# Performance work log

Hardware: AMD Instinct MI355X
Metric: run time of the kernel (lower is better)

## Reference

```python
import jax, jax.numpy as jnp
import numpy as np

B, N, M, C = 4, 4096, 300, 1152
SA_H, SA_D = 36, 32           # linear self-attention heads / head dim
CA_H = 16                     # cross-attention heads
INNER_SA = SA_H * SA_D        # 1152
INNER_FF = int(C * 2.5)       # 2880
EPS = 1e-6


def _ln(x):
    # LayerNorm without affine, eps=1e-6
    mu = x.mean(-1, keepdims=True)
    var = x.var(-1, keepdims=True)
    return (x - mu) / jnp.sqrt(var + EPS)


def setup_inputs() -> dict:
    key = jax.random.key(0)
    ks = jax.random.split(key, 24)
    p = lambda i, shape: jax.random.normal(ks[i], shape, jnp.float32) * 0.02
    return {
        "x": jax.random.normal(ks[0], (B, N, C), jnp.float32),
        "conditioning": jax.random.normal(ks[1], (B, M, C), jnp.float32),
        "t_emb": jax.random.normal(ks[2], (B, C), jnp.float32),
        # linear self-attention (qkv has no bias)
        "w_qkv": p(3, (C, 3 * INNER_SA)),
        "w_sa_out": p(4, (INNER_SA, C)),
        "b_sa_out": jnp.zeros((C,), jnp.float32),
        # norm_cross (affine LayerNorm)
        "gamma_cross": jnp.ones((C,), jnp.float32),
        "beta_cross": jnp.zeros((C,), jnp.float32),
        # cross-attention
        "w_q": p(5, (C, C)), "b_q": jnp.zeros((C,), jnp.float32),
        "w_kv": p(6, (C, 2 * C)), "b_kv": jnp.zeros((2 * C,), jnp.float32),
        "w_co": p(7, (C, C)), "b_co": jnp.zeros((C,), jnp.float32),
        # MixFFN
        "w_fc1": p(8, (C, 2 * INNER_FF)), "b_fc1": jnp.zeros((2 * INNER_FF,), jnp.float32),
        "dw_kernel": p(9, (3, 3, 1, INNER_FF)),  # depthwise conv, HWIO
        "dw_bias": jnp.zeros((INNER_FF,), jnp.float32),
        "w_fc2": p(10, (INNER_FF, C)), "b_fc2": jnp.zeros((C,), jnp.float32),
        # adaLN modulation
        "w_ada": p(11, (C, 6 * C)), "b_ada": jnp.zeros((6 * C,), jnp.float32),
        "sst": jax.random.normal(ks[12], (6, C), jnp.float32) * 0.02,
    }


def reference(x, conditioning, t_emb, w_qkv, w_sa_out, b_sa_out,
              gamma_cross, beta_cross, w_q, b_q, w_kv, b_kv, w_co, b_co,
              w_fc1, b_fc1, dw_kernel, dw_bias, w_fc2, b_fc2,
              w_ada, b_ada, sst):
    Bx, Nx, Cx = x.shape
    ada = jax.nn.silu(t_emb) @ w_ada + b_ada          # (B, 6C)
    ada = sst[None] + ada.reshape(Bx, 6, Cx)          # (B, 6, C)
    shift_sa, scale_sa, gate_sa, shift_ff, scale_ff, gate_ff = (
        ada[:, 0], ada[:, 1], ada[:, 2], ada[:, 3], ada[:, 4], ada[:, 5])

    # --- modulated linear self-attention (ReLU kernel) ---
    xn = _ln(x) * (1.0 + scale_sa[:, None]) + shift_sa[:, None]
    qkv = (xn @ w_qkv).reshape(Bx, Nx, 3, SA_H, SA_D)
    q = jax.nn.relu(qkv[:, :, 0])
    k = jax.nn.relu(qkv[:, :, 1])
    v = qkv[:, :, 2]
    kv = jnp.einsum('bnhd,bnhe->bhde', k, v)                  # (B,H,D,D)
    out = jnp.einsum('bnhd,bhde->bnhe', q, kv)                # (B,N,H,D)
    denom = jnp.einsum('bnhd,bhd->bnh', q, k.sum(1)) + 1e-6   # (B,N,H)
    out = (out / denom[..., None]).reshape(Bx, Nx, INNER_SA)
    x = x + gate_sa[:, None] * (out @ w_sa_out + b_sa_out)

    # --- cross-attention (softmax) ---
    xc = _ln(x) * gamma_cross + beta_cross
    hd = Cx // CA_H
    qc = (xc @ w_q + b_q).reshape(Bx, Nx, CA_H, hd)
    kvc = (conditioning @ w_kv + b_kv).reshape(Bx, M, 2, CA_H, hd)
    kc, vc = kvc[:, :, 0], kvc[:, :, 1]
    attn = jnp.einsum('bnhd,bmhd->bhnm', qc, kc) * (hd ** -0.5)
    attn = jax.nn.softmax(attn, axis=-1)
    oc = jnp.einsum('bhnm,bmhd->bnhd', attn, vc).reshape(Bx, Nx, Cx)
    x = x + oc @ w_co + b_co

    # --- modulated GLU-dwconv FFN ---
    xn = _ln(x) * (1.0 + scale_ff[:, None]) + shift_ff[:, None]
    gv = xn @ w_fc1 + b_fc1
    gate, val = gv[..., :INNER_FF], gv[..., INNER_FF:]
    h = jax.nn.silu(gate) * val
    hw = int(round(Nx ** 0.5))
    h = h.reshape(Bx, hw, hw, INNER_FF)                       # NHWC
    h = jax.lax.conv_general_dilated(
        h, dw_kernel, window_strides=(1, 1), padding='SAME',
        dimension_numbers=('NHWC', 'HWIO', 'NHWC'),
        feature_group_count=INNER_FF) + dw_bias
    h = h.reshape(Bx, Nx, INNER_FF)
    x = x + gate_ff[:, None] * (h @ w_fc2 + b_fc2)
    return x
```

## Files before the change

### kernel.cpp

```cpp
#include <hip/hip_runtime.h>

typedef __bf16 bf16_t;
typedef __attribute__((ext_vector_type(8))) __bf16 bf16x8;
typedef __attribute__((ext_vector_type(4))) __bf16 bf16x4;
typedef __attribute__((ext_vector_type(4))) float f32x4;

#define DEVINL __device__ __forceinline__

DEVINL void gload16(const void* g, void* l) {
  __builtin_amdgcn_global_load_lds(
      (const __attribute__((address_space(1))) void*)g,
      (__attribute__((address_space(3))) void*)l, 16, 0, 0);
}

template <int OUT>
__global__ __launch_bounds__(512) void gemm256r(
    const bf16_t* __restrict__ A, const bf16_t* __restrict__ Bt,
    void* __restrict__ Cv, int M, int N, int K,
    const float* __restrict__ bias, const float* __restrict__ resid,
    const float* __restrict__ gate, int GM)
{
  __shared__ __align__(16) bf16_t sL[3][2][256 * 32];
  const int tid = threadIdx.x;
  const int lane = tid & 63;
  const int wave = tid >> 6;
  const int wr = wave >> 2;
  const int wc = wave & 3;

  const int nbx = gridDim.x, nby = gridDim.y;
  const int nwg = nbx * nby;
  int lin = (int)blockIdx.y * nbx + (int)blockIdx.x;
  {
    const int q = nwg >> 3, rr = nwg & 7;
    const int xcd = lin & 7, idx = lin >> 3;
    lin = (xcd < rr ? xcd * (q + 1) : rr * (q + 1) + (xcd - rr) * q) + idx;
  }
  const int per_grp = GM * nbx;
  const int gid = lin / per_grp;
  const int rem = lin - gid * per_grp;
  const int gsz = min(GM, nby - gid * GM);
  const long tileM = (long)(gid * GM + rem % gsz) * 256;
  const long tileN = (long)(rem / gsz) * 256;

  const int r0 = tid >> 2;
  const int c0 = (((tid & 3) - (r0 >> 2)) & 3) * 8;

  auto STAGE = [&](int slot, int kt) {
    const bf16_t* ga = A + (tileM + r0) * (long)K + kt + c0;
    const bf16_t* gb = Bt + (tileN + r0) * (long)K + kt + c0;
    char* la = (char*)&sL[slot][0][0] + tid * 16;
    char* lb = (char*)&sL[slot][1][0] + tid * 16;
    gload16(ga, la);
    gload16(ga + 128 * (long)K, la + 8192);
    gload16(gb, lb);
    gload16(gb + 128 * (long)K, lb + 8192);
  };

  f32x4 acc[8][4] = {};
  const int NT = K >> 5;

  STAGE(0, 0); STAGE(1, 32); STAGE(2, 64);
  asm volatile("s_waitcnt vmcnt(8)" ::: "memory");
  asm volatile("s_barrier" ::: "memory");

  const int r = lane & 15;
  const int kg = lane >> 4;
  const int sw = ((kg + (r >> 2)) & 3) * 16;
  const int abyte = (wr * 128 + r) * 64 + sw;
  const int bbyte = (wc * 64 + r) * 64 + sw;

  int slot = 0;
  for (int t = 0; t < NT; ++t) {
    const char* pA = (const char*)&sL[slot][0][0];
    const char* pB = (const char*)&sL[slot][1][0];
    bf16x8 a[8], b[4];
#pragma unroll
    for (int n = 0; n < 4; ++n) b[n] = *(const bf16x8*)(pB + bbyte + n * 1024);
#pragma unroll
    for (int m = 0; m < 8; ++m) a[m] = *(const bf16x8*)(pA + abyte + m * 1024);
    __builtin_amdgcn_s_setprio(1);
#pragma unroll
    for (int m = 0; m < 8; ++m)
#pragma unroll
      for (int n = 0; n < 4; ++n)
        acc[m][n] = __builtin_amdgcn_mfma_f32_16x16x32_bf16(a[m], b[n],
                                                            acc[m][n], 0, 0, 0);
    __builtin_amdgcn_s_setprio(0);
    if (t + 1 >= NT) break;
    if (t + 2 < NT) asm volatile("s_waitcnt vmcnt(4)" ::: "memory");
    else            asm volatile("s_waitcnt vmcnt(0)" ::: "memory");
    asm volatile("s_barrier" ::: "memory");
    if (t + 3 < NT) STAGE(slot, (t + 3) << 5);
    slot = (slot == 2) ? 0 : slot + 1;
  }

  const long row0 = tileM + wr * 128 + ((lane >> 4) * 4);
  const int col0 = (int)tileN + wc * 64 + r;
#pragma unroll
  for (int m = 0; m < 8; ++m) {
#pragma unroll
    for (int n = 0; n < 4; ++n) {
      const int col = col0 + n * 16;
      if (col < N) {
        const float bb = bias ? bias[col] : 0.0f;
#pragma unroll
        for (int j = 0; j < 4; ++j) {
          const long row = row0 + m * 16 + j;
          const long idx = row * (long)N + col;
          const float v = acc[m][n][j] + bb;
          if constexpr (OUT == 1) {
            const float g = gate ? gate[(row >> 12) * 6912 + col] : 1.0f;
            const float rv = resid ? resid[idx] : 0.0f;
            ((float*)Cv)[idx] = rv + g * v;
          } else {
            ((bf16_t*)Cv)[idx] = (bf16_t)v;
          }
        }
      }
    }
  }
}

template <int OUT>
__global__ __launch_bounds__(256) void gemm_bt(
    const bf16_t* __restrict__ A, const bf16_t* __restrict__ Bt,
    void* __restrict__ Cv, int M, int N, int K,
    long strideA, long strideB, long strideC,
    const float* __restrict__ bias, const float* __restrict__ resid,
    const float* __restrict__ gate, int GM)
{
  __shared__ __align__(16) bf16_t sA[128 * 32];
  __shared__ __align__(16) bf16_t sB[128 * 32];
  const int tid = threadIdx.x;
  const int lane = tid & 63;
  const int wave = tid >> 6;
  const bf16_t* Ab = A + (size_t)blockIdx.z * strideA;
  const bf16_t* Bb = Bt + (size_t)blockIdx.z * strideB;

  const int nbx = gridDim.x, nby = gridDim.y;
  const int nwg = nbx * nby;
  int lin = (int)blockIdx.y * nbx + (int)blockIdx.x;
  {
    const int q = nwg >> 3, rr = nwg & 7;
    const int xcd = lin & 7, idx = lin >> 3;
    lin = (xcd < rr ? xcd * (q + 1) : rr * (q + 1) + (xcd - rr) * q) + idx;
  }
  const int per_grp = GM * nbx;
  const int gid = lin / per_grp;
  const int rem = lin - gid * per_grp;
  const int gsz = min(GM, nby - gid * GM);
  const long tileM = (long)(gid * GM + rem % gsz) * 128;
  const long tileN = (long)(rem / gsz) * 128;
  const int wr = wave >> 1, wc = wave & 1;

  f32x4 acc[4][4] = {};

  const int srow = lane >> 2;
  const int skcol = (lane & 3) * 8;
  const bf16_t* gA0 = Ab + (tileM + wave * 16 + srow) * (long)K + skcol;
  const bf16_t* gB0 = Bb + (tileN + wave * 16 + srow) * (long)K + skcol;
  bf16_t* lA0 = sA + wave * 512;
  bf16_t* lB0 = sB + wave * 512;
  const long rs64 = 64L * K;

  const int aoff = (wr * 64 + (lane & 15)) * 32 + (lane >> 4) * 8;
  const int boff = (wc * 64 + (lane & 15)) * 32 + (lane >> 4) * 8;

  for (int kt = 0; kt < K; kt += 32) {
    __syncthreads();
    gload16(gA0 + kt, lA0);
    gload16(gA0 + kt + rs64, lA0 + 2048);
    gload16(gB0 + kt, lB0);
    gload16(gB0 + kt + rs64, lB0 + 2048);
    __syncthreads();
    bf16x8 av[4], bv[4];
#pragma unroll
    for (int m = 0; m < 4; ++m) av[m] = *(const bf16x8*)&sA[aoff + m * 512];
#pragma unroll
    for (int n = 0; n < 4; ++n) bv[n] = *(const bf16x8*)&sB[boff + n * 512];
#pragma unroll
    for (int m = 0; m < 4; ++m)
#pragma unroll
      for (int n = 0; n < 4; ++n)
        acc[m][n] = __builtin_amdgcn_mfma_f32_16x16x32_bf16(av[m], bv[n],
                                                            acc[m][n], 0, 0, 0);
  }

  const long row0 = tileM + wr * 64 + ((lane >> 4) * 4);
  const int col0 = (int)tileN + wc * 64 + (lane & 15);
#pragma unroll
  for (int m = 0; m < 4; ++m) {
#pragma unroll
    for (int n = 0; n < 4; ++n) {
      const int col = col0 + n * 16;
      const float bb = (OUT != 2 && bias) ? bias[col] : 0.0f;
#pragma unroll
      for (int j = 0; j < 4; ++j) {
        const long row = row0 + m * 16 + j;
        const float v = acc[m][n][j] + bb;
        if constexpr (OUT == 1) {
          const long idx = row * (long)N + col;
          const float g = gate ? gate[(row >> 12) * 6912 + col] : 1.0f;
          const float rv = resid ? resid[idx] : 0.0f;
          ((float*)Cv)[idx] = rv + g * v;
        } else if constexpr (OUT == 2) {
          if (col < 72)
            ((bf16_t*)Cv)[(((long)(blockIdx.z >> 4)) * 4096 + row) * 1152 +
                          (long)(blockIdx.z & 15) * 72 + col] = (bf16_t)v;
        } else {
          const long idx = row * (long)N + col;
          (((bf16_t*)Cv) + (size_t)blockIdx.z * strideC)[idx] = (bf16_t)v;
        }
      }
    }
  }
}

__global__ __launch_bounds__(256) void transpose_cast(
    const float* __restrict__ W, bf16_t* __restrict__ WT, int K, int N)
{
  __shared__ float tile[32][33];
  const int n0 = blockIdx.x * 32, k0 = blockIdx.y * 32;
  const int tx = threadIdx.x & 31, ty = threadIdx.x >> 5;
#pragma unroll
  for (int r = ty; r < 32; r += 8) tile[r][tx] = W[(size_t)(k0 + r) * N + n0 + tx];
  __syncthreads();
#pragma unroll
  for (int r = ty; r < 32; r += 8)
    WT[(size_t)(n0 + r) * K + k0 + tx] = (bf16_t)tile[tx][r];
}

__global__ __launch_bounds__(256) void ada_kernel(
    const float* __restrict__ t_emb, const float* __restrict__ w_ada,
    const float* __restrict__ b_ada, const float* __restrict__ sst,
    float* __restrict__ ada)
{
  __shared__ float st[4][1152];
  const int t = threadIdx.x;
  const int j = blockIdx.x * 256 + t;
  for (int i = t; i < 4 * 1152; i += 256) {
    const int b = i / 1152, cc = i % 1152;
    const float v = t_emb[b * 1152 + cc];
    st[b][cc] = v / (1.0f + __expf(-v));
  }
  __syncthreads();
  const int k0 = blockIdx.y * 144;
  float a0 = 0.f, a1 = 0.f, a2 = 0.f, a3 = 0.f;
  for (int k = k0; k < k0 + 144; ++k) {
    const float w = w_ada[(size_t)k * 6912 + j];
    a0 += st[0][k] * w; a1 += st[1][k] * w;
    a2 += st[2][k] * w; a3 += st[3][k] * w;
  }
  if (blockIdx.y == 0) {
    const float base = b_ada[j] + sst[j];
    a0 += base; a1 += base; a2 += base; a3 += base;
  }
  atomicAdd(&ada[0 * 6912 + j], a0);
  atomicAdd(&ada[1 * 6912 + j], a1);
  atomicAdd(&ada[2 * 6912 + j], a2);
  atomicAdd(&ada[3 * 6912 + j], a3);
}

__global__ __launch_bounds__(256) void ln_mod(
    const float* __restrict__ X, bf16_t* __restrict__ out,
    const float* __restrict__ adaB, int shiftIdx, int scaleIdx,
    const float* __restrict__ gamma, const float* __restrict__ beta)
{
  const int row = blockIdx.x;
  const float4* xr4 = (const float4*)(X + (size_t)row * 1152);
  float s = 0.f, s2 = 0.f;
  for (int i = threadIdx.x; i < 288; i += 256) {
    const float4 v = xr4[i];
    s += v.x + v.y + v.z + v.w;
    s2 += v.x * v.x + v.y * v.y + v.z * v.z + v.w * v.w;
  }
  const int lane = threadIdx.x & 63, wave = threadIdx.x >> 6;
#pragma unroll
  for (int o = 32; o; o >>= 1) { s += __shfl_down(s, o); s2 += __shfl_down(s2, o); }
  __shared__ float rs[4], rq[4];
  if (lane == 0) { rs[wave] = s; rq[wave] = s2; }
  __syncthreads();
  if (threadIdx.x == 0) {
    rs[0] = rs[0] + rs[1] + rs[2] + rs[3];
    rq[0] = rq[0] + rq[1] + rq[2] + rq[3];
  }
  __syncthreads();
  const float mu = rs[0] * (1.0f / 1152.0f);
  const float var = rq[0] * (1.0f / 1152.0f) - mu * mu;
  const float inv = rsqrtf(var + 1e-6f);
  const int b = row >> 12;
  const float4* shiftv = (const float4*)(adaB ? adaB + b * 6912 + shiftIdx * 1152 : beta);
  const float4* scalev = (const float4*)(adaB ? adaB + b * 6912 + scaleIdx * 1152 : gamma);
  const float add1 = adaB ? 1.0f : 0.0f;
  for (int i = threadIdx.x; i < 288; i += 256) {
    const float4 v = xr4[i];
    const float4 sc = scalev[i];
    const float4 sh = shiftv[i];
    bf16x4 o;
    o[0] = (bf16_t)((v.x - mu) * inv * (add1 + sc.x) + sh.x);
    o[1] = (bf16_t)((v.y - mu) * inv * (add1 + sc.y) + sh.y);
    o[2] = (bf16_t)((v.z - mu) * inv * (add1 + sc.z) + sh.z);
    o[3] = (bf16_t)((v.w - mu) * inv * (add1 + sc.w) + sh.w);
    *(bf16x4*)&out[(size_t)row * 1152 + i * 4] = o;
  }
}

__global__ void pad_cond_k(const float* __restrict__ cond, bf16_t* __restrict__ condp)
{
  const int idx = blockIdx.x * 256 + threadIdx.x;
  const int row = idx / 1152;
  condp[idx] = (row < 1200) ? (bf16_t)cond[idx] : (bf16_t)0.0f;
}

__global__ __launch_bounds__(256) void sa_kv_k(
    const bf16_t* __restrict__ qkv, float* __restrict__ kvb, float* __restrict__ ksumb)
{
  const int bh = blockIdx.x, b = bh / 36, h = bh % 36;
  __shared__ bf16_t sk[32][32], sv[32][32];
  const int t = threadIdx.x;
  const int nn = t >> 5, c = t & 31;
  const int srow = (t & 127) >> 2;
  const int sq4 = (t & 3) * 8;
  const int isV = t >> 7;
  float a0 = 0.f, a1 = 0.f, a2 = 0.f, a3 = 0.f, ks = 0.f;
  const size_t rowbase = (size_t)b * 4096 + (size_t)blockIdx.y * 256;
  const size_t colbase = 1152 + (size_t)isV * 1152 + h * 32 + sq4;
  for (int n0 = 0; n0 < 256; n0 += 32) {
    __syncthreads();
    const bf16x8 v8 = *(const bf16x8*)&qkv[(rowbase + n0 + srow) * 3456 + colbase];
    if (isV == 0) {
      bf16x8 r8;
#pragma unroll
      for (int j = 0; j < 8; ++j) r8[j] = (bf16_t)fmaxf((float)v8[j], 0.0f);
      *(bf16x8*)&sk[srow][sq4] = r8;
    } else {
      *(bf16x8*)&sv[srow][sq4] = v8;
    }
    __syncthreads();
#pragma unroll
    for (int q = 0; q < 32; ++q) {
      const float vv = (float)sv[q][c];
      a0 += (float)sk[q][nn] * vv;
      a1 += (float)sk[q][nn + 8] * vv;
      a2 += (float)sk[q][nn + 16] * vv;
      a3 += (float)sk[q][nn + 24] * vv;
    }
    if (t < 32) {
#pragma unroll
      for (int q = 0; q < 32; ++q) ks += (float)sk[q][t];
    }
  }
  float* kvp = kvb + (size_t)bh * 1024;
  atomicAdd(&kvp[(nn + 0) * 32 + c], a0);
  atomicAdd(&kvp[(nn + 8) * 32 + c], a1);
  atomicAdd(&kvp[(nn + 16) * 32 + c], a2);
  atomicAdd(&kvp[(nn + 24) * 32 + c], a3);
  if (t < 32) atomicAdd(&ksumb[bh * 32 + t], ks);
}

__global__ __launch_bounds__(256) void sa_out_k(
    const bf16_t* __restrict__ qkv, const float* __restrict__ kvb,
    const float* __restrict__ ksumb, bf16_t* __restrict__ so)
{
  const int row0 = blockIdx.x * 8;
  const int b = row0 >> 12;
  __shared__ float q[8][1152];
  __shared__ float denom[8][36];
  const int t = threadIdx.x;
  for (int i = t; i < 1152; i += 256) {
    const int r = i / 144, c0 = (i % 144) * 8;
    const bf16x8 v8 = *(const bf16x8*)&qkv[(size_t)(row0 + r) * 3456 + c0];
#pragma unroll
    for (int j = 0; j < 8; ++j) q[r][c0 + j] = fmaxf((float)v8[j], 0.0f);
  }
  __syncthreads();
  for (int i = t; i < 288; i += 256) {
    int r = i / 36, h = i % 36;
    const float* ksp = ksumb + (b * 36 + h) * 32;
    float dsum = 1e-6f;
#pragma unroll
    for (int d = 0; d < 32; ++d) dsum += q[r][h * 32 + d] * ksp[d];
    denom[r][h] = dsum;
  }
  __syncthreads();
  for (int j = t; j < 1152; j += 256) {
    const int h = j >> 5, e = j & 31;
    const float* kvp = kvb + ((size_t)(b * 36 + h)) * 1024 + e;
    float kreg[32];
#pragma unroll
    for (int d = 0; d < 32; ++d) kreg[d] = kvp[d * 32];
#pragma unroll
    for (int r = 0; r < 8; ++r) {
      float a = 0.f;
#pragma unroll
      for (int d = 0; d < 32; ++d) a += q[r][h * 32 + d] * kreg[d];
      so[(size_t)(row0 + r) * 1152 + j] = (bf16_t)(a / denom[r][h]);
    }
  }
}

__global__ void ca_qrepack(const bf16_t* __restrict__ qc, bf16_t* __restrict__ qcp, int b)
{
  const size_t idx = (size_t)blockIdx.x * 256 + threadIdx.x;
  const int d = (int)(idx % 96);
  const size_t r = idx / 96;
  const int n = (int)(r & 4095);
  const int h = (int)(r >> 12);
  float v = 0.f;
  if (d < 72) v = (float)qc[((size_t)(b * 4096 + n)) * 1152 + h * 72 + d] * 0.11785113019775793f;
  qcp[idx] = (bf16_t)v;
}

__global__ void ca_kcrepack(const bf16_t* __restrict__ kvc, bf16_t* __restrict__ kcp, int b)
{
  const size_t idx = (size_t)blockIdx.x * 256 + threadIdx.x;
  const int d = (int)(idx % 96);
  const size_t r = idx / 96;
  const int m = (int)(r % 384);
  const int h = (int)(r / 384);
  bf16_t v = (bf16_t)0.0f;
  if (d < 72 && m < 300) v = kvc[((size_t)(b * 300 + m)) * 2304 + h * 72 + d];
  kcp[idx] = v;
}

__global__ void ca_vtrepack(const bf16_t* __restrict__ kvc, bf16_t* __restrict__ vt, int b)
{
  const size_t idx = (size_t)blockIdx.x * 256 + threadIdx.x;
  const int m = (int)(idx % 384);
  const size_t r = idx / 384;
  const int d = (int)(r & 127);
  const int h = (int)(r >> 7);
  bf16_t v = (bf16_t)0.0f;
  if (d < 72 && m < 300) v = kvc[((size_t)(b * 300 + m)) * 2304 + 1152 + h * 72 + d];
  vt[idx] = v;
}

__global__ __launch_bounds__(256) void softmax_k(bf16_t* __restrict__ s)
{
  const int row = blockIdx.x * 4 + (threadIdx.x >> 6);
  const int lane = threadIdx.x & 63;
  bf16_t* sr = s + (size_t)row * 384;
  float v[5];
  float mx = -1e30f;
#pragma unroll
  for (int i = 0; i < 5; ++i) {
    const int m = lane + 64 * i;
    v[i] = (m < 300) ? (float)sr[m] : -1e30f;
    mx = fmaxf(mx, v[i]);
  }
#pragma unroll
  for (int o = 32; o; o >>= 1) mx = fmaxf(mx, __shfl_xor(mx, o));
  float sum = 0.f;
#pragma unroll
  for (int i = 0; i < 5; ++i) { v[i] = __expf(v[i] - mx); sum += v[i]; }
#pragma unroll
  for (int o = 32; o; o >>= 1) sum += __shfl_xor(sum, o);
  const float inv = 1.0f / sum;
#pragma unroll
  for (int i = 0; i < 5; ++i) {
    const int m = lane + 64 * i;
    if (m < 320) sr[m] = (bf16_t)(v[i] * inv);
  }
}

__global__ void glu_k(const bf16_t* __restrict__ gv, bf16_t* __restrict__ h)
{
  const size_t idx = (size_t)blockIdx.x * 256 + threadIdx.x;
  const size_t row = idx / 360;
  const int c0 = (int)(idx % 360) * 8;
  const bf16x8 g8 = *(const bf16x8*)&gv[row * 5760 + c0];
  const bf16x8 v8 = *(const bf16x8*)&gv[row * 5760 + 2880 + c0];
  bf16x8 o;
#pragma unroll
  for (int j = 0; j < 8; ++j) {
    const float g = (float)g8[j];
    const float sg = g / (1.0f + __expf(-g));
    o[j] = (bf16_t)(sg * (float)v8[j]);
  }
  *(bf16x8*)&h[row * 2880 + c0] = o;
}

__global__ __launch_bounds__(256) void dwconv_k(
    const bf16_t* __restrict__ h, const float* __restrict__ wk,
    const float* __restrict__ wb, bf16_t* __restrict__ hc)
{
  const size_t idx = (size_t)blockIdx.x * 256 + threadIdx.x;
  const int c8 = (int)(idx % 360);
  size_t p = idx / 360;
  const int x = (int)(p & 63);
  const int y = (int)(p >> 6);
  const int c0 = c8 * 8;
  float acc[8];
#pragma unroll
  for (int j = 0; j < 8; ++j) acc[j] = wb[c0 + j];
  for (int ky = -1; ky <= 1; ++ky) {
    const int yy = y + ky;
    if (yy < 0 || yy > 63) continue;
    for (int kx = -1; kx <= 1; ++kx) {
      const int xx = x + kx;
      if (xx < 0 || xx > 63) continue;
      const bf16x8 v = *(const bf16x8*)&h[((size_t)(yy * 64 + xx)) * 2880 + c0];
      const float* w = wk + ((ky + 1) * 3 + (kx + 1)) * 2880 + c0;
#pragma unroll
      for (int j = 0; j < 8; ++j) acc[j] += (float)v[j] * w[j];
    }
  }
  bf16x8 o;
#pragma unroll
  for (int j = 0; j < 8; ++j) o[j] = (bf16_t)acc[j];
  *(bf16x8*)&hc[((size_t)(y * 64 + x)) * 2880 + c0] = o;
}

extern "C" void kernel_launch(void* const* d_in, const int* in_sizes, int n_in,
                              void* d_out, int out_size, void* d_ws, size_t ws_size,
                              hipStream_t stream)
{
  const float* x          = (const float*)d_in[0];
  const float* cond       = (const float*)d_in[1];
  const float* t_emb      = (const float*)d_in[2];
  const float* w_qkv      = (const float*)d_in[3];
  const float* w_sa_out   = (const float*)d_in[4];
  const float* b_sa_out   = (const float*)d_in[5];
  const float* gamma_cr   = (const float*)d_in[6];
  const float* beta_cr    = (const float*)d_in[7];
  const float* w_q        = (const float*)d_in[8];
  const float* b_q        = (const float*)d_in[9];
  const float* w_kv       = (const float*)d_in[10];
  const float* b_kv       = (const float*)d_in[11];
  const float* w_co       = (const float*)d_in[12];
  const float* b_co       = (const float*)d_in[13];
  const float* w_fc1      = (const float*)d_in[14];
  const float* b_fc1      = (const float*)d_in[15];
  const float* dw_kernel  = (const float*)d_in[16];
  const float* dw_bias    = (const float*)d_in[17];
  const float* w_fc2      = (const float*)d_in[18];
  const float* b_fc2      = (const float*)d_in[19];
  const float* w_ada      = (const float*)d_in[20];
  const float* b_ada      = (const float*)d_in[21];
  const float* sst        = (const float*)d_in[22];
  float* out = (float*)d_out;

  char* ws = (char*)d_ws;
  size_t off = 0;
  auto alloc = [&](size_t bytes) -> char* {
    off = (off + 255) & ~(size_t)255;
    char* p = ws + off;
    off += bytes;
    return p;
  };

  bf16_t* wqkvT  = (bf16_t*)alloc((size_t)3584 * 1152 * 2);
  bf16_t* wsaT   = (bf16_t*)alloc((size_t)1280 * 1152 * 2);
  bf16_t* wqT    = (bf16_t*)alloc((size_t)1280 * 1152 * 2);
  bf16_t* wkvT   = (bf16_t*)alloc((size_t)2304 * 1152 * 2);
  bf16_t* wcoT   = (bf16_t*)alloc((size_t)1280 * 1152 * 2);
  bf16_t* wfc1T  = (bf16_t*)alloc((size_t)5888 * 1152 * 2);
  bf16_t* wfc2T  = (bf16_t*)alloc((size_t)1280 * 2880 * 2);
  float*  adaB   = (float*)alloc((size_t)4 * 6912 * 4);
  bf16_t* xn     = (bf16_t*)alloc((size_t)16384 * 1152 * 2);
  bf16_t* buf37  = (bf16_t*)alloc((size_t)16384 * 1152 * 2);
  float*  kvb    = (float*)alloc((size_t)144 * 1024 * 4);
  float*  ksumb  = (float*)alloc((size_t)144 * 32 * 4);
  bf16_t* condp  = (bf16_t*)alloc((size_t)1280 * 1152 * 2);
  bf16_t* kvcB   = (bf16_t*)alloc((size_t)1280 * 2304 * 2);

  const size_t ARENA_SMALL = (size_t)16384 * 3456 * 2;
  const size_t CA_Q = (size_t)64 * 4096 * 96 * 2;
  const size_t CA_K = (size_t)64 * 384 * 96 * 2;
  const size_t CA_V = (size_t)64 * 128 * 384 * 2;
  const size_t CA_S = (size_t)64 * 4096 * 384 * 2;
  const size_t ARENA_BIG = CA_Q + CA_K + CA_V + CA_S;
  const bool big = (off + 512 + ARENA_BIG) <= ws_size;
  char* arena = alloc(big ? ARENA_BIG : ARENA_SMALL);
  if (off > ws_size) return;

  bf16_t* qkvB = (bf16_t*)arena;
  bf16_t *qcp, *kcp, *vcT, *scores;
  if (big) {
    qcp    = (bf16_t*)arena;
    kcp    = (bf16_t*)(arena + CA_Q);
    vcT    = (bf16_t*)(arena + CA_Q + CA_K);
    scores = (bf16_t*)(arena + CA_Q + CA_K + CA_V);
  } else {
    qcp    = (bf16_t*)arena;
    kcp    = (bf16_t*)(arena + 12582912);
    vcT    = (bf16_t*)(arena + 12582912 + 1179648);
    scores = (bf16_t*)(arena + 12582912 + 1179648 + 1572864);
  }
  bf16_t *gvB, *hB, *hcB;
  if (big) {
    gvB = (bf16_t*)arena;
    hB  = (bf16_t*)(arena + (size_t)8192 * 5760 * 2);
    hcB = (bf16_t*)(arena + (size_t)8192 * 5760 * 2 + (size_t)8192 * 2880 * 2);
  } else {
    hcB = (bf16_t*)arena;
    gvB = (bf16_t*)(arena + (size_t)8192 * 2880 * 2);
    hB  = buf37;
  }

  hipMemsetAsync(adaB, 0, (size_t)4 * 6912 * 4, stream);
  hipMemsetAsync(kvb, 0, (size_t)144 * 1024 * 4, stream);
  hipMemsetAsync(ksumb, 0, (size_t)144 * 32 * 4, stream);

  transpose_cast<<<dim3(108, 36), 256, 0, stream>>>(w_qkv, wqkvT, 1152, 3456);
  transpose_cast<<<dim3(36, 36), 256, 0, stream>>>(w_sa_out, wsaT, 1152, 1152);
  transpose_cast<<<dim3(36, 36), 256, 0, stream>>>(w_q, wqT, 1152, 1152);
  transpose_cast<<<dim3(72, 36), 256, 0, stream>>>(w_kv, wkvT, 1152, 2304);
  transpose_cast<<<dim3(36, 36), 256, 0, stream>>>(w_co, wcoT, 1152, 1152);
  transpose_cast<<<dim3(180, 36), 256, 0, stream>>>(w_fc1, wfc1T, 1152, 5760);
  transpose_cast<<<dim3(36, 90), 256, 0, stream>>>(w_fc2, wfc2T, 2880, 1152);
  ada_kernel<<<dim3(27, 8), 256, 0, stream>>>(t_emb, w_ada, b_ada, sst, adaB);
  pad_cond_k<<<5760, 256, 0, stream>>>(cond, condp);

  ln_mod<<<16384, 256, 0, stream>>>(x, xn, adaB, 0, 1, nullptr, nullptr);
  gemm256r<0><<<dim3(14, 64), 512, 0, stream>>>(xn, wqkvT, qkvB, 16384, 3456, 1152,
                                                nullptr, nullptr, nullptr, 8);
  sa_kv_k<<<dim3(144, 16), 256, 0, stream>>>(qkvB, kvb, ksumb);
  sa_out_k<<<2048, 256, 0, stream>>>(qkvB, kvb, ksumb, buf37);
  gemm_bt<1><<<dim3(9, 128), 256, 0, stream>>>(buf37, wsaT, out, 16384, 1152, 1152,
                                               0, 0, 0, b_sa_out, x, adaB + 2 * 1152, 8);

  ln_mod<<<16384, 256, 0, stream>>>(out, xn, nullptr, 0, 0, gamma_cr, beta_cr);
  gemm_bt<0><<<dim3(9, 128), 256, 0, stream>>>(xn, wqT, buf37, 16384, 1152, 1152,
                                               0, 0, 0, b_q, nullptr, nullptr, 8);
  gemm_bt<0><<<dim3(18, 10, 1), 256, 0, stream>>>(condp, wkvT, kvcB, 1280, 2304, 1152,
                                                  0, 0, 0, b_kv, nullptr, nullptr, 8);
  if (big) {
    for (int b = 0; b < 4; ++b) {
      ca_qrepack<<<24576, 256, 0, stream>>>(buf37, qcp + (size_t)b * 16 * 4096 * 96, b);
      ca_kcrepack<<<2304, 256, 0, stream>>>(kvcB, kcp + (size_t)b * 16 * 384 * 96, b);
      ca_vtrepack<<<3072, 256, 0, stream>>>(kvcB, vcT + (size_t)b * 16 * 128 * 384, b);
    }
    gemm_bt<0><<<dim3(3, 32, 64), 256, 0, stream>>>(qcp, kcp, scores, 4096, 384, 96,
                                                    (long)4096 * 96, (long)384 * 96,
                                                    (long)4096 * 384, nullptr, nullptr, nullptr, 8);
    softmax_k<<<65536, 256, 0, stream>>>(scores);
    gemm_bt<2><<<dim3(1, 32, 64), 256, 0, stream>>>(scores, vcT, buf37, 4096, 128, 384,
                                                    (long)4096 * 384, (long)128 * 384,
                                                    0, nullptr, nullptr, nullptr, 8);
  } else {
    for (int b = 0; b < 4; ++b) {
      ca_qrepack<<<24576, 256, 0, stream>>>(buf37, qcp, b);
      ca_kcrepack<<<2304, 256, 0, stream>>>(kvcB, kcp, b);
      ca_vtrepack<<<3072, 256, 0, stream>>>(kvcB, vcT, b);
      gemm_bt<0><<<dim3(3, 32, 16), 256, 0, stream>>>(qcp, kcp, scores, 4096, 384, 96,
                                                      (long)4096 * 96, (long)384 * 96,
                                                      (long)4096 * 384, nullptr, nullptr, nullptr, 8);
      softmax_k<<<16384, 256, 0, stream>>>(scores);
      gemm_bt<2><<<dim3(1, 32, 16), 256, 0, stream>>>(scores, vcT,
                                                      buf37 + (size_t)b * 4096 * 1152,
                                                      4096, 128, 384,
                                                      (long)4096 * 384, (long)128 * 384,
                                                      0, nullptr, nullptr, nullptr, 8);
    }
  }
  gemm_bt<1><<<dim3(9, 128), 256, 0, stream>>>(buf37, wcoT, out, 16384, 1152, 1152,
                                               0, 0, 0, b_co, out, nullptr, 8);

  ln_mod<<<16384, 256, 0, stream>>>(out, xn, adaB, 3, 4, nullptr, nullptr);
  if (big) {
    for (int c = 0; c < 2; ++c) {
      gemm256r<0><<<dim3(23, 32), 512, 0, stream>>>(xn + (size_t)c * 8192 * 1152, wfc1T,
                                                    gvB, 8192, 5760, 1152,
                                                    b_fc1, nullptr, nullptr, 8);
      glu_k<<<11520, 256, 0, stream>>>(gvB, hB);
      for (int bb = 0; bb < 2; ++bb)
        dwconv_k<<<5760, 256, 0, stream>>>(hB + (size_t)bb * 4096 * 2880,
                                           dw_kernel, dw_bias,
                                           hcB + (size_t)bb * 4096 * 2880);
      gemm_bt<1><<<dim3(9, 64), 256, 0, stream>>>(hcB, wfc2T,
                                                  out + (size_t)c * 8192 * 1152,
                                                  8192, 1152, 2880, 0, 0, 0, b_fc2,
                                                  out + (size_t)c * 8192 * 1152,
                                                  adaB + (size_t)c * 2 * 6912 + 5 * 1152, 8);
    }
  } else {
    for (int c = 0; c < 2; ++c) {
      for (int bb = 0; bb < 2; ++bb) {
        const int b = c * 2 + bb;
        gemm256r<0><<<dim3(23, 16), 512, 0, stream>>>(xn + (size_t)b * 4096 * 1152, wfc1T,
                                                      gvB, 4096, 5760, 1152,
                                                      b_fc1, nullptr, nullptr, 8);
        glu_k<<<5760, 256, 0, stream>>>(gvB, hB);
        dwconv_k<<<5760, 256, 0, stream>>>(hB, dw_kernel, dw_bias,
                                           hcB + (size_t)bb * 4096 * 2880);
      }
      gemm_bt<1><<<dim3(9, 64), 256, 0, stream>>>(hcB, wfc2T,
                                                  out + (size_t)c * 8192 * 1152,
                                                  8192, 1152, 2880, 0, 0, 0, b_fc2,
                                                  out + (size_t)c * 8192 * 1152,
                                                  adaB + (size_t)c * 2 * 6912 + 5 * 1152, 8);
    }
  }

  (void)in_sizes; (void)n_in; (void)out_size; (void)ws_size;
}
```

Measured before the change: 1.856 ms.

## Fuse cross-attn Q repack into GEMM epilogue, double-buffer gemm256r, batch fc2

The Q-projection GEMM gets a new epilogue mode that writes its output directly in the padded per-head layout, pre-scaled by the attention scale. This removes the separate ca_qrepack launches and the intermediate buffer round trip on the big path, at the cost of an extra memset of the padded Q buffer. gemm256r goes from triple to double buffering in LDS, which lowers shared-memory use but waits for all loads to finish each iteration, so less copy time is hidden behind compute. The fc2 GEMM on the big path now runs once over all 16384 rows instead of twice over halves, which needs hcB to hold the full conv output.

```diff
diff --git a/kernel.cpp b/kernel.cpp
--- a/kernel.cpp
+++ b/kernel.cpp
@@ -20,7 +20,7 @@
     const float* __restrict__ bias, const float* __restrict__ resid,
     const float* __restrict__ gate, int GM)
 {
-  __shared__ __align__(16) bf16_t sL[3][2][256 * 32];
+  __shared__ __align__(16) bf16_t sL[2][2][256 * 32];
   const int tid = threadIdx.x;
   const int lane = tid & 63;
   const int wave = tid >> 6;
@@ -59,8 +59,8 @@
   f32x4 acc[8][4] = {};
   const int NT = K >> 5;
 
-  STAGE(0, 0); STAGE(1, 32); STAGE(2, 64);
-  asm volatile("s_waitcnt vmcnt(8)" ::: "memory");
+  STAGE(0, 0); STAGE(1, 32);
+  asm volatile("s_waitcnt vmcnt(4)" ::: "memory");
   asm volatile("s_barrier" ::: "memory");
 
   const int r = lane & 15;
@@ -69,10 +69,9 @@
   const int abyte = (wr * 128 + r) * 64 + sw;
   const int bbyte = (wc * 64 + r) * 64 + sw;
 
-  int slot = 0;
   for (int t = 0; t < NT; ++t) {
-    const char* pA = (const char*)&sL[slot][0][0];
-    const char* pB = (const char*)&sL[slot][1][0];
+    const char* pA = (const char*)&sL[t & 1][0][0];
+    const char* pB = (const char*)&sL[t & 1][1][0];
     bf16x8 a[8], b[4];
 #pragma unroll
     for (int n = 0; n < 4; ++n) b[n] = *(const bf16x8*)(pB + bbyte + n * 1024);
@@ -87,11 +86,9 @@
                                                             acc[m][n], 0, 0, 0);
     __builtin_amdgcn_s_setprio(0);
     if (t + 1 >= NT) break;
-    if (t + 2 < NT) asm volatile("s_waitcnt vmcnt(4)" ::: "memory");
-    else            asm volatile("s_waitcnt vmcnt(0)" ::: "memory");
+    asm volatile("s_waitcnt vmcnt(0)" ::: "memory");
     asm volatile("s_barrier" ::: "memory");
-    if (t + 3 < NT) STAGE(slot, (t + 3) << 5);
-    slot = (slot == 2) ? 0 : slot + 1;
+    if (t + 2 < NT) STAGE(t & 1, (t + 2) << 5);
   }
 
   const long row0 = tileM + wr * 128 + ((lane >> 4) * 4);
@@ -207,6 +204,11 @@
           if (col < 72)
             ((bf16_t*)Cv)[(((long)(blockIdx.z >> 4)) * 4096 + row) * 1152 +
                           (long)(blockIdx.z & 15) * 72 + col] = (bf16_t)v;
+        } else if constexpr (OUT == 3) {
+          const int h = col / 72, d = col - h * 72;
+          const long b = row >> 12, n4 = row & 4095;
+          ((bf16_t*)Cv)[((b * 16 + h) * 4096 + n4) * 96 + d] =
+              (bf16_t)(v * 0.11785113019775793f);
         } else {
           const long idx = row * (long)N + col;
           (((bf16_t*)Cv) + (size_t)blockIdx.z * strideC)[idx] = (bf16_t)v;
@@ -621,13 +623,13 @@
                                                0, 0, 0, b_sa_out, x, adaB + 2 * 1152, 8);
 
   ln_mod<<<16384, 256, 0, stream>>>(out, xn, nullptr, 0, 0, gamma_cr, beta_cr);
-  gemm_bt<0><<<dim3(9, 128), 256, 0, stream>>>(xn, wqT, buf37, 16384, 1152, 1152,
-                                               0, 0, 0, b_q, nullptr, nullptr, 8);
   gemm_bt<0><<<dim3(18, 10, 1), 256, 0, stream>>>(condp, wkvT, kvcB, 1280, 2304, 1152,
                                                   0, 0, 0, b_kv, nullptr, nullptr, 8);
   if (big) {
+    hipMemsetAsync(qcp, 0, CA_Q, stream);
+    gemm_bt<3><<<dim3(9, 128), 256, 0, stream>>>(xn, wqT, qcp, 16384, 1152, 1152,
+                                                 0, 0, 0, b_q, nullptr, nullptr, 8);
     for (int b = 0; b < 4; ++b) {
-      ca_qrepack<<<24576, 256, 0, stream>>>(buf37, qcp + (size_t)b * 16 * 4096 * 96, b);
       ca_kcrepack<<<2304, 256, 0, stream>>>(kvcB, kcp + (size_t)b * 16 * 384 * 96, b);
       ca_vtrepack<<<3072, 256, 0, stream>>>(kvcB, vcT + (size_t)b * 16 * 128 * 384, b);
     }
@@ -639,6 +641,8 @@
                                                     (long)4096 * 384, (long)128 * 384,
                                                     0, nullptr, nullptr, nullptr, 8);
   } else {
+    gemm_bt<0><<<dim3(9, 128), 256, 0, stream>>>(xn, wqT, buf37, 16384, 1152, 1152,
+                                                 0, 0, 0, b_q, nullptr, nullptr, 8);
     for (int b = 0; b < 4; ++b) {
       ca_qrepack<<<24576, 256, 0, stream>>>(buf37, qcp, b);
       ca_kcrepack<<<2304, 256, 0, stream>>>(kvcB, kcp, b);
@@ -667,13 +671,11 @@
       for (int bb = 0; bb < 2; ++bb)
         dwconv_k<<<5760, 256, 0, stream>>>(hB + (size_t)bb * 4096 * 2880,
                                            dw_kernel, dw_bias,
-                                           hcB + (size_t)bb * 4096 * 2880);
-      gemm_bt<1><<<dim3(9, 64), 256, 0, stream>>>(hcB, wfc2T,
-                                                  out + (size_t)c * 8192 * 1152,
-                                                  8192, 1152, 2880, 0, 0, 0, b_fc2,
-                                                  out + (size_t)c * 8192 * 1152,
-                                                  adaB + (size_t)c * 2 * 6912 + 5 * 1152, 8);
-    }
+                                           hcB + (size_t)(c * 2 + bb) * 4096 * 2880);
+    }
+    gemm_bt<1><<<dim3(9, 128), 256, 0, stream>>>(hcB, wfc2T, out, 16384, 1152, 2880,
+                                                 0, 0, 0, b_fc2, out,
+                                                 adaB + 5 * 1152, 8);
   } else {
     for (int c = 0; c < 2; ++c) {
       for (int bb = 0; bb < 2; ++bb) {
```

Measured after the change: 1.891 ms. No clear change (+1.9%).
